# Performance work log

Hardware: AMD Instinct MI355X
Metric: run time of the kernel (lower is better)

Reference implementation:

```python
import jax, jax.numpy as jnp
import numpy as np

NEG_SLOPE = 0.2  # PyG GATConv default leaky_relu slope


def _gat_layer(x, src, dst, N, W, a_src, a_dst, b):
    # x: [N, Fin] -> h: [N, Fout]
    h = x @ W
    e_src = h @ a_src  # [N]
    e_dst = h @ a_dst  # [N]
    # per-edge attention logit, edge j->i uses src=j, dst=i
    e = jax.nn.leaky_relu(e_src[src] + e_dst[dst], NEG_SLOPE)  # [E]
    # segment softmax over incoming edges of each dst node
    m = jax.ops.segment_max(e, dst, num_segments=N)            # [N]
    ex = jnp.exp(e - m[dst])
    denom = jax.ops.segment_sum(ex, dst, num_segments=N)       # [N]
    alpha = ex / denom[dst]                                    # [E]
    out = jax.ops.segment_sum(alpha[:, None] * h[src], dst, num_segments=N)
    return out + b


def setup_inputs() -> dict:
    key = jax.random.key(0)
    ks = jax.random.split(key, 10)
    N, E_CNT, F_IN, F_HID, F_OUT = 100000, 3200000, 512, 8, 32
    E = jax.random.randint(ks[0], (2, E_CNT), 0, N, dtype=jnp.int64)
    X = jax.random.normal(ks[1], (N, F_IN), dtype=jnp.float32)
    s = 0.05
    return {
        "V": N,
        "E": E,
        "X": X,
        "W1": jax.random.normal(ks[2], (F_IN, F_HID), jnp.float32) * s,
        "a1_src": jax.random.normal(ks[3], (F_HID,), jnp.float32) * s,
        "a1_dst": jax.random.normal(ks[4], (F_HID,), jnp.float32) * s,
        "b1": jnp.zeros((F_HID,), jnp.float32),
        "W2": jax.random.normal(ks[5], (F_HID, F_OUT), jnp.float32) * s,
        "a2_src": jax.random.normal(ks[6], (F_OUT,), jnp.float32) * s,
        "a2_dst": jax.random.normal(ks[7], (F_OUT,), jnp.float32) * s,
        "b2": jnp.zeros((F_OUT,), jnp.float32),
    }


def reference(V, E, X, W1, a1_src, a1_dst, b1, W2, a2_src, a2_dst, b2):
    N = X.shape[0]
    # add_self_loops=True inside each GATConv
    loops = jnp.arange(N, dtype=E.dtype)
    src = jnp.concatenate([E[0], loops])
    dst = jnp.concatenate([E[1], loops])
    # dropout(p=0.6) is identity in eval mode
    h1 = jax.nn.elu(_gat_layer(X, src, dst, N, W1, a1_src, a1_dst, b1))
    out = _gat_layer(h1, src, dst, N, W2, a2_src, a2_dst, b2)
    return out
```

## Files before the change

kernel.cpp:

```cpp
#include <hip/hip_runtime.h>
#include <hip/hip_fp16.h>
#include <math.h>

#define F_IN 512
#define NEG_SLOPE 0.2f
#define CAPG 10240
#define SCAT_BLKS 768
#define CHUNK_MAX 4304
#define GEMM_BLKS 1536
#define NBUK_MAX 400

#define STG_OFF  0
#define LCNT_OFF (CHUNK_MAX)
#define LOFS_OFF (LCNT_OFF + 400)
#define GOFS_OFF (LOFS_OFF + 404)
#define WS_OFF   (GOFS_OFF + 400)
#define SMEM_INTS (WS_OFF + 8)

template <int CTRL>
__device__ __forceinline__ float dpp_row_add(float v) {
    int t = __builtin_amdgcn_update_dpp(0, __float_as_int(v), CTRL, 0xF, 0xF, true);
    return v + __int_as_float(t);
}
__device__ __forceinline__ float reduce16(float v) {
    v = dpp_row_add<0xB1>(v);
    v = dpp_row_add<0x4E>(v);
    v = dpp_row_add<0x124>(v);
    v = dpp_row_add<0x128>(v);
    return v;
}

__global__ __launch_bounds__(256) void k_main(
    const float* __restrict__ X, const float* __restrict__ W1,
    const float* __restrict__ a1s, const float* __restrict__ a1d,
    const float* __restrict__ W2, const float* __restrict__ a2s,
    const float* __restrict__ a2d,
    const int* __restrict__ E, int EC, int N,
    int* __restrict__ cursor, unsigned* __restrict__ bucketArr,
    char* __restrict__ rec1, float* __restrict__ e1d,
    float* __restrict__ wa2s, float* __restrict__ wa2d)
{
    __shared__ __align__(16) int smem[SMEM_INTS];
    int tid = threadIdx.x;
    int lane = tid & 63;
    int wv = tid >> 6;

    if (blockIdx.x < SCAT_BLKS) {
        unsigned* stage = (unsigned*)(smem + STG_OFF);
        int* lcnt = smem + LCNT_OFF;
        int* lofs = smem + LOFS_OFF;
        int* gofs = smem + GOFS_OFF;
        int* wsum = smem + WS_OFF;

        int odd = E[2 * lane + 1];
        unsigned long long bl = __ballot(odd == 0);
        int w64 = (bl == ~0ULL) ? 1 : 0;
        const int* srcBase = E;
        const int* dstBase = w64 ? (E + 2 * (size_t)EC) : (E + (size_t)EC);
        int step = w64 ? 2 : 1;
        int total = EC + N;
        int nb = (N + 255) >> 8;
        int chunk = (total + SCAT_BLKS - 1) / SCAT_BLKS;
        int e0 = blockIdx.x * chunk;
        int e1 = min(e0 + chunk, total);
        int cnt = max(e1 - e0, 0);

        for (int i = tid; i < NBUK_MAX; i += 256) lcnt[i] = 0;
        __syncthreads();
        for (int e = e0 + tid; e < e1; e += 256) {
            int d = (e < EC) ? dstBase[(size_t)e * step] : (e - EC);
            atomicAdd(&lcnt[d >> 8], 1);
        }
        __syncthreads();
        int b0 = tid * 2;
        int s0 = (b0 < nb) ? lcnt[b0] : 0;
        int s1 = (b0 + 1 < nb) ? lcnt[b0 + 1] : 0;
        int tsum = s0 + s1;
        int sc = tsum;
#pragma unroll
        for (int off = 1; off < 64; off <<= 1) {
            int t = __shfl_up(sc, off, 64);
            if (lane >= off) sc += t;
        }
        if (lane == 63) wsum[wv] = sc;
        __syncthreads();
        if (tid == 0) { int run = 0; for (int i = 0; i < 4; ++i) { int t = wsum[i]; wsum[i] = run; run += t; } }
        __syncthreads();
        int texc = wsum[wv] + sc - tsum;
        if (b0 < nb) lofs[b0] = texc;
        if (b0 + 1 < nb) lofs[b0 + 1] = texc + s0;
        if (tid == 0) lofs[nb] = cnt;
        __syncthreads();
        for (int b = tid; b < nb; b += 256) {
            int c = lcnt[b];
            gofs[b] = (c ? atomicAdd(&cursor[b], c) : 0) - lofs[b];
        }
        __syncthreads();
        for (int i = tid; i < NBUK_MAX; i += 256) lcnt[i] = 0;
        __syncthreads();
        for (int e = e0 + tid; e < e1; e += 256) {
            int s, d;
            if (e < EC) { s = srcBase[(size_t)e * step]; d = dstBase[(size_t)e * step]; }
            else        { s = e - EC; d = s; }
            int b = d >> 8;
            int r = atomicAdd(&lcnt[b], 1);
            stage[lofs[b] + r] = ((unsigned)(d & 255) << 24) | (unsigned)s;
        }
        __syncthreads();
        int WIN = (cnt + 3) >> 2;
        int wstart = wv * WIN;
        int wend = min(wstart + WIN, cnt);
        int i = wstart + lane;
        int p = 0;
        if (i < wend) {
            int lo = 0, hi = nb - 1;
            while (lo < hi) {
                int mid = (lo + hi + 1) >> 1;
                if (lofs[mid] <= i) lo = mid; else hi = mid - 1;
            }
            p = lo;
        }
        for (; i < wend; i += 64) {
            while (p + 1 < nb && lofs[p + 1] <= i) ++p;
            bucketArr[(size_t)p * CAPG + gofs[p] + i] = stage[i];
        }
    } else if (blockIdx.x < SCAT_BLKS + GEMM_BLKS) {
        float* rw = (float*)smem + wv * 680;

        float Wk[8][8];
        const float4* W4 = (const float4*)W1;
#pragma unroll
        for (int i = 0; i < 8; ++i) {
            int k = lane + 64 * i;
            float4 w0 = W4[k * 2], w1 = W4[k * 2 + 1];
            Wk[i][0]=w0.x; Wk[i][1]=w0.y; Wk[i][2]=w0.z; Wk[i][3]=w0.w;
            Wk[i][4]=w1.x; Wk[i][5]=w1.y; Wk[i][6]=w1.z; Wk[i][7]=w1.w;
        }
        float was[8], wad[8];
#pragma unroll
        for (int i = 0; i < 8; ++i) {
            float ts = 0.f, td = 0.f;
#pragma unroll
            for (int j = 0; j < 8; ++j) { ts += Wk[i][j] * a1s[j]; td += Wk[i][j] * a1d[j]; }
            was[i] = ts; wad[i] = td;
        }

        const int stride = GEMM_BLKS * 4;
        int row = (blockIdx.x - SCAT_BLKS) * 4 + wv;
        if (row >= N) return;
        float x[8], xn[8];
        {
            const float* xr = X + (size_t)row * F_IN + lane;
#pragma unroll
            for (int i = 0; i < 8; ++i) x[i] = xr[64 * i];
        }
        int j10 = lane & 15, c16 = lane >> 4;
        while (row < N) {
            int nrow = row + stride;
            if (nrow < N) {
                const float* xq = X + (size_t)nrow * F_IN + lane;
#pragma unroll
                for (int i = 0; i < 8; ++i) xn[i] = xq[64 * i];
            }
            float acc[8];
#pragma unroll
            for (int j = 0; j < 8; ++j) {
                float t = x[0] * Wk[0][j];
#pragma unroll
                for (int i = 1; i < 8; ++i) t += x[i] * Wk[i][j];
                acc[j] = t;
            }
            float accs = 0.f, accd = 0.f;
#pragma unroll
            for (int i = 0; i < 8; ++i) { accs += x[i] * was[i]; accd += x[i] * wad[i]; }
#pragma unroll
            for (int j = 0; j < 8; ++j) rw[j * 68 + lane] = acc[j];
            rw[8 * 68 + lane] = accs;
            rw[9 * 68 + lane] = accd;
            float s = 0.f;
            if (j10 < 10) {
                const float4* pr = (const float4*)&rw[j10 * 68 + c16 * 16];
                float4 q0 = pr[0], q1 = pr[1], q2 = pr[2], q3 = pr[3];
                s = ((q0.x+q0.y)+(q0.z+q0.w)) + ((q1.x+q1.y)+(q1.z+q1.w))
                  + ((q2.x+q2.y)+(q2.z+q2.w)) + ((q3.x+q3.y)+(q3.z+q3.w));
            }
            s += __shfl_xor(s, 16, 64);
            s += __shfl_xor(s, 32, 64);
            float hp = __shfl_xor(s, 1, 64);
            if (lane < 10) {
                char* rp = rec1 + (size_t)row * 32;
                if (lane < 8) {
                    if ((lane & 1) == 0)
                        *(__half2*)(rp + (lane >> 1) * 4) = __floats2half2_rn(s, hp);
                } else if (lane == 8) {
                    *(float*)(rp + 16) = s;
                } else {
                    e1d[row] = s;
                }
            }
            row = nrow;
#pragma unroll
            for (int i = 0; i < 8; ++i) x[i] = xn[i];
        }
    } else {
        if (tid < 8) {
            float s = 0.f;
            for (int j = 0; j < 32; ++j) s += W2[tid * 32 + j] * a2s[j];
            wa2s[tid] = s;
        } else if (tid < 16) {
            int k = tid - 8;
            float s = 0.f;
            for (int j = 0; j < 32; ++j) s += W2[k * 32 + j] * a2d[j];
            wa2d[k] = s;
        }
    }
}

__global__ __launch_bounds__(256) void k_csr_build(
    unsigned* __restrict__ bucketArr, const int* __restrict__ cursor,
    int2* __restrict__ offs2, int N)
{
    __shared__ int deg[256];
    __shared__ int wsum[4];
    __shared__ int stage[CAPG];
    int b = blockIdx.x;
    unsigned* ba = bucketArr + (size_t)b * CAPG;
    int cnt = min(cursor[b], CAPG);
    int bbase = b * CAPG;
    int nodeBase = b << 8;
    int nNodes = min(256, N - nodeBase);
    int tid = threadIdx.x;
    deg[tid] = 0;
    __syncthreads();
    for (int e = tid; e < cnt; e += 256)
        atomicAdd(&deg[ba[e] >> 24], 1);
    __syncthreads();
    int lane = tid & 63, wid = tid >> 6;
    int v = deg[tid];
    int s = v;
#pragma unroll
    for (int off = 1; off < 64; off <<= 1) {
        int t = __shfl_up(s, off, 64);
        if (lane >= off) s += t;
    }
    if (lane == 63) wsum[wid] = s;
    __syncthreads();
    if (tid == 0) { int run = 0; for (int i = 0; i < 4; ++i) { int t = wsum[i]; wsum[i] = run; run += t; } }
    __syncthreads();
    int ex = wsum[wid] + s - v;
    if (tid < nNodes) offs2[nodeBase + tid] = make_int2(bbase + ex, bbase + ex + v);
    __syncthreads();
    deg[tid] = ex;
    __syncthreads();
    for (int e = tid; e < cnt; e += 256) {
        unsigned pv = ba[e];
        int pos = atomicAdd(&deg[pv >> 24], 1);
        stage[pos] = (int)(pv & 0xFFFFFFu);
    }
    __syncthreads();
    for (int e = tid; e < cnt; e += 256)
        ba[e] = (unsigned)stage[e];
}

__global__ __launch_bounds__(256) void k_agg1(
    const int2* __restrict__ offs2, const unsigned* __restrict__ csr,
    const char* __restrict__ rec1, const float* __restrict__ e1d,
    const float* __restrict__ b1, const float* __restrict__ wa2s,
    const float* __restrict__ wa2d,
    char* __restrict__ rec2, float* __restrict__ e2d, int N)
{
    __shared__ float sb1[8], sws[8], swd[8];
    if (threadIdx.x < 8) sb1[threadIdx.x] = b1[threadIdx.x];
    else if (threadIdx.x < 16) sws[threadIdx.x - 8] = wa2s[threadIdx.x - 8];
    else if (threadIdx.x < 24) swd[threadIdx.x - 16] = wa2d[threadIdx.x - 16];
    __syncthreads();

    int lane = threadIdx.x & 63;
    int sub = (lane & 15) | ((lane >> 5) << 4);
    int g = (lane >> 4) & 1;
    int n = blockIdx.x * 8 + ((threadIdx.x >> 6) << 1) + g;
    if (n >= N) return;

    int2 be = offs2[n];
    int beg = be.x, end = be.y;
    float edn = e1d[n];
    float den = 0.f;
    float acc[8];
#pragma unroll
    for (int k = 0; k < 8; ++k) acc[k] = 0.f;

    for (int e = beg + sub; e < end; e += 32) {
        int s = (int)csr[e];
        const char* rp = rec1 + (size_t)s * 32;
        uint4 u = *(const uint4*)rp;
        float esv = *(const float*)(rp + 16);
        float t = esv + edn;
        t = fmaxf(t, NEG_SLOPE * t);
        float ex = __expf(fminf(t, 80.f));
        den += ex;
        float2 f0 = __half22float2(*(__half2*)&u.x);
        float2 f1 = __half22float2(*(__half2*)&u.y);
        float2 f2 = __half22float2(*(__half2*)&u.z);
        float2 f3 = __half22float2(*(__half2*)&u.w);
        acc[0] += ex * f0.x; acc[1] += ex * f0.y; acc[2] += ex * f1.x; acc[3] += ex * f1.y;
        acc[4] += ex * f2.x; acc[5] += ex * f2.y; acc[6] += ex * f3.x; acc[7] += ex * f3.y;
    }
    den = reduce16(den); den += __shfl_xor(den, 32, 64);
#pragma unroll
    for (int k = 0; k < 8; ++k) {
        acc[k] = reduce16(acc[k]);
        acc[k] += __shfl_xor(acc[k], 32, 64);
    }

    float inv = 1.f / den;
    float o[8]; float s2 = 0.f, d2 = 0.f;
#pragma unroll
    for (int k = 0; k < 8; ++k) {
        float t = acc[k] * inv + sb1[k];
        t = t > 0.f ? t : expm1f(t);
        o[k] = t; s2 += t * sws[k]; d2 += t * swd[k];
    }
    if (sub == 0) {
        __half2 p0 = __floats2half2_rn(o[0], o[1]);
        __half2 p1 = __floats2half2_rn(o[2], o[3]);
        __half2 p2 = __floats2half2_rn(o[4], o[5]);
        __half2 p3 = __floats2half2_rn(o[6], o[7]);
        uint4 u; u.x = *(unsigned*)&p0; u.y = *(unsigned*)&p1;
                 u.z = *(unsigned*)&p2; u.w = *(unsigned*)&p3;
        char* rp = rec2 + (size_t)n * 32;
        *(uint4*)rp = u;
        *(float*)(rp + 16) = s2;
        e2d[n] = d2;
    }
}

__global__ __launch_bounds__(256) void k_agg2(
    const int2* __restrict__ offs2, const unsigned* __restrict__ csr,
    const char* __restrict__ rec2, const float* __restrict__ e2d,
    const float* __restrict__ W2, const float* __restrict__ b2,
    float* __restrict__ out, int N)
{
    __shared__ float sW[256], sb[32];
    sW[threadIdx.x] = W2[threadIdx.x];
    if (threadIdx.x < 32) sb[threadIdx.x] = b2[threadIdx.x];
    __syncthreads();

    int lane = threadIdx.x & 63;
    int sub = (lane & 15) | ((lane >> 5) << 4);
    int g = (lane >> 4) & 1;
    int n = blockIdx.x * 8 + ((threadIdx.x >> 6) << 1) + g;
    if (n >= N) return;

    int2 be = offs2[n];
    int beg = be.x, end = be.y;
    float edn = e2d[n];
    float den = 0.f;
    float acc[8];
#pragma unroll
    for (int k = 0; k < 8; ++k) acc[k] = 0.f;

    for (int e = beg + sub; e < end; e += 32) {
        int s = (int)csr[e];
        const char* rp = rec2 + (size_t)s * 32;
        uint4 u = *(const uint4*)rp;
        float esv = *(const float*)(rp + 16);
        float t = esv + edn;
        t = fmaxf(t, NEG_SLOPE * t);
        float ex = __expf(fminf(t, 80.f));
        den += ex;
        float2 f0 = __half22float2(*(__half2*)&u.x);
        float2 f1 = __half22float2(*(__half2*)&u.y);
        float2 f2 = __half22float2(*(__half2*)&u.z);
        float2 f3 = __half22float2(*(__half2*)&u.w);
        acc[0] += ex * f0.x; acc[1] += ex * f0.y; acc[2] += ex * f1.x; acc[3] += ex * f1.y;
        acc[4] += ex * f2.x; acc[5] += ex * f2.y; acc[6] += ex * f3.x; acc[7] += ex * f3.y;
    }
    den = reduce16(den); den += __shfl_xor(den, 32, 64);
#pragma unroll
    for (int k = 0; k < 8; ++k) {
        acc[k] = reduce16(acc[k]);
        acc[k] += __shfl_xor(acc[k], 32, 64);
    }

    float inv = 1.f / den;
    float o = 0.f;
#pragma unroll
    for (int k = 0; k < 8; ++k) o += (acc[k] * inv) * sW[k * 32 + sub];
    out[(size_t)n * 32 + sub] = o + sb[sub];
}

extern "C" void kernel_launch(void* const* d_in, const int* in_sizes, int n_in,
                              void* d_out, int out_size, void* d_ws, size_t ws_size,
                              hipStream_t stream)
{
    const int*   E   = (const int*)d_in[1];
    const float* X   = (const float*)d_in[2];
    const float* W1  = (const float*)d_in[3];
    const float* a1s = (const float*)d_in[4];
    const float* a1d = (const float*)d_in[5];
    const float* b1  = (const float*)d_in[6];
    const float* W2  = (const float*)d_in[7];
    const float* a2s = (const float*)d_in[8];
    const float* a2d = (const float*)d_in[9];
    const float* b2  = (const float*)d_in[10];

    int N  = in_sizes[2] / F_IN;
    int EC = in_sizes[1] / 2;
    int NB = (N + 255) >> 8;

    char* w = (char*)d_ws;
    auto take = [&](size_t bytes) { char* p = w; w += (bytes + 255) & ~(size_t)255; return p; };

    char*  rec1 = take((size_t)N * 32);
    char*  rec2 = take((size_t)N * 32);
    float* e1d  = (float*)take((size_t)N * 4);
    float* e2d  = (float*)take((size_t)N * 4);
    unsigned* bucketArr = (unsigned*)take((size_t)NBUK_MAX * CAPG * 4);
    int2*  offs2 = (int2*)take((size_t)N * 8);
    int*   cursor = (int*)take(NBUK_MAX * 4);
    float* wa2s = (float*)take(256);
    float* wa2d = (float*)take(256);

    (void)hipMemsetAsync(cursor, 0, NBUK_MAX * 4, stream);

    k_main<<<SCAT_BLKS + GEMM_BLKS + 1, 256, 0, stream>>>(
        X, W1, a1s, a1d, W2, a2s, a2d, E, EC, N,
        cursor, bucketArr, rec1, e1d, wa2s, wa2d);

    k_csr_build<<<NB, 256, 0, stream>>>(bucketArr, cursor, offs2, N);

    int blocks8 = (N + 7) / 8;
    k_agg1<<<blocks8, 256, 0, stream>>>(offs2, bucketArr, rec1, e1d, b1, wa2s, wa2d,
                                        rec2, e2d, N);
    k_agg2<<<blocks8, 256, 0, stream>>>(offs2, bucketArr, rec2, e2d, W2, b2,
                                        (float*)d_out, N);
}
```

Baseline: 161.2 us.

## Fuse CSR build with layer-1 aggregation using shared-memory staged edges

The CSR build kernel and the layer-1 aggregation kernel are merged into one 512-thread kernel per 256-node bucket. After sorting edges into shared memory, each node is aggregated by a pair of threads that read source ids straight from the shared stage buffer. This removes a kernel launch and the global re-read of CSR indices and offsets. In exchange, parallelism per node drops from 32 lanes to 2, so high-degree nodes and load imbalance could lengthen the aggregation phase, and occupancy is limited by the large shared buffer.

```diff
diff --git a/kernel.cpp b/kernel.cpp
--- a/kernel.cpp
+++ b/kernel.cpp
@@ -216,13 +216,19 @@
     }
 }
 
-__global__ __launch_bounds__(256) void k_csr_build(
+__global__ __launch_bounds__(512) void k_csr_agg1(
     unsigned* __restrict__ bucketArr, const int* __restrict__ cursor,
-    int2* __restrict__ offs2, int N)
+    int2* __restrict__ offs2,
+    const char* __restrict__ rec1, const float* __restrict__ e1d,
+    const float* __restrict__ b1, const float* __restrict__ wa2s,
+    const float* __restrict__ wa2d,
+    char* __restrict__ rec2, float* __restrict__ e2d, int N)
 {
     __shared__ int deg[256];
+    __shared__ int begS[256];
     __shared__ int wsum[4];
     __shared__ int stage[CAPG];
+    __shared__ float sb1[8], sws[8], swd[8];
     int b = blockIdx.x;
     unsigned* ba = bucketArr + (size_t)b * CAPG;
     int cnt = min(cursor[b], CAPG);
@@ -230,103 +236,91 @@
     int nodeBase = b << 8;
     int nNodes = min(256, N - nodeBase);
     int tid = threadIdx.x;
-    deg[tid] = 0;
-    __syncthreads();
-    for (int e = tid; e < cnt; e += 256)
+
+    if (tid < 256) deg[tid] = 0;
+    else if (tid < 264) sb1[tid - 256] = b1[tid - 256];
+    else if (tid < 272) sws[tid - 264] = wa2s[tid - 264];
+    else if (tid < 280) swd[tid - 272] = wa2d[tid - 272];
+    __syncthreads();
+    for (int e = tid; e < cnt; e += 512)
         atomicAdd(&deg[ba[e] >> 24], 1);
     __syncthreads();
     int lane = tid & 63, wid = tid >> 6;
-    int v = deg[tid];
-    int s = v;
-#pragma unroll
-    for (int off = 1; off < 64; off <<= 1) {
-        int t = __shfl_up(s, off, 64);
-        if (lane >= off) s += t;
-    }
-    if (lane == 63) wsum[wid] = s;
+    int v = 0, s = 0;
+    if (tid < 256) {
+        v = deg[tid];
+        s = v;
+#pragma unroll
+        for (int off = 1; off < 64; off <<= 1) {
+            int t = __shfl_up(s, off, 64);
+            if (lane >= off) s += t;
+        }
+        if (lane == 63) wsum[wid] = s;
+    }
     __syncthreads();
     if (tid == 0) { int run = 0; for (int i = 0; i < 4; ++i) { int t = wsum[i]; wsum[i] = run; run += t; } }
     __syncthreads();
-    int ex = wsum[wid] + s - v;
-    if (tid < nNodes) offs2[nodeBase + tid] = make_int2(bbase + ex, bbase + ex + v);
-    __syncthreads();
-    deg[tid] = ex;
-    __syncthreads();
-    for (int e = tid; e < cnt; e += 256) {
+    if (tid < 256) {
+        int ex = wsum[wid] + s - v;
+        begS[tid] = ex;
+        if (tid < nNodes) offs2[nodeBase + tid] = make_int2(bbase + ex, bbase + ex + v);
+    }
+    __syncthreads();
+    if (tid < 256) deg[tid] = begS[tid];
+    __syncthreads();
+    for (int e = tid; e < cnt; e += 512) {
         unsigned pv = ba[e];
         int pos = atomicAdd(&deg[pv >> 24], 1);
         stage[pos] = (int)(pv & 0xFFFFFFu);
     }
     __syncthreads();
-    for (int e = tid; e < cnt; e += 256)
+    for (int e = tid; e < cnt; e += 512)
         ba[e] = (unsigned)stage[e];
-}
-
-__global__ __launch_bounds__(256) void k_agg1(
-    const int2* __restrict__ offs2, const unsigned* __restrict__ csr,
-    const char* __restrict__ rec1, const float* __restrict__ e1d,
-    const float* __restrict__ b1, const float* __restrict__ wa2s,
-    const float* __restrict__ wa2d,
-    char* __restrict__ rec2, float* __restrict__ e2d, int N)
-{
-    __shared__ float sb1[8], sws[8], swd[8];
-    if (threadIdx.x < 8) sb1[threadIdx.x] = b1[threadIdx.x];
-    else if (threadIdx.x < 16) sws[threadIdx.x - 8] = wa2s[threadIdx.x - 8];
-    else if (threadIdx.x < 24) swd[threadIdx.x - 16] = wa2d[threadIdx.x - 16];
-    __syncthreads();
-
-    int lane = threadIdx.x & 63;
-    int sub = (lane & 15) | ((lane >> 5) << 4);
-    int g = (lane >> 4) & 1;
-    int n = blockIdx.x * 8 + ((threadIdx.x >> 6) << 1) + g;
-    if (n >= N) return;
-
-    int2 be = offs2[n];
-    int beg = be.x, end = be.y;
-    float edn = e1d[n];
+    int node = tid >> 1, half = tid & 1;
     float den = 0.f;
     float acc[8];
 #pragma unroll
     for (int k = 0; k < 8; ++k) acc[k] = 0.f;
-
-    for (int e = beg + sub; e < end; e += 32) {
-        int s = (int)csr[e];
-        const char* rp = rec1 + (size_t)s * 32;
-        uint4 u = *(const uint4*)rp;
-        float esv = *(const float*)(rp + 16);
-        float t = esv + edn;
-        t = fmaxf(t, NEG_SLOPE * t);
-        float ex = __expf(fminf(t, 80.f));
-        den += ex;
-        float2 f0 = __half22float2(*(__half2*)&u.x);
-        float2 f1 = __half22float2(*(__half2*)&u.y);
-        float2 f2 = __half22float2(*(__half2*)&u.z);
-        float2 f3 = __half22float2(*(__half2*)&u.w);
-        acc[0] += ex * f0.x; acc[1] += ex * f0.y; acc[2] += ex * f1.x; acc[3] += ex * f1.y;
-        acc[4] += ex * f2.x; acc[5] += ex * f2.y; acc[6] += ex * f3.x; acc[7] += ex * f3.y;
-    }
-    den = reduce16(den); den += __shfl_xor(den, 32, 64);
-#pragma unroll
-    for (int k = 0; k < 8; ++k) {
-        acc[k] = reduce16(acc[k]);
-        acc[k] += __shfl_xor(acc[k], 32, 64);
-    }
-
-    float inv = 1.f / den;
-    float o[8]; float s2 = 0.f, d2 = 0.f;
-#pragma unroll
-    for (int k = 0; k < 8; ++k) {
-        float t = acc[k] * inv + sb1[k];
-        t = t > 0.f ? t : expm1f(t);
-        o[k] = t; s2 += t * sws[k]; d2 += t * swd[k];
-    }
-    if (sub == 0) {
+    if (node < nNodes) {
+        int beg = begS[node], end = deg[node];
+        float edn = e1d[nodeBase + node];
+        for (int e = beg + half; e < end; e += 2) {
+            int src = stage[e];
+            const char* rp = rec1 + (size_t)src * 32;
+            uint4 u = *(const uint4*)rp;
+            float esv = *(const float*)(rp + 16);
+            float t = esv + edn;
+            t = fmaxf(t, NEG_SLOPE * t);
+            float ex = __expf(fminf(t, 80.f));
+            den += ex;
+            float2 f0 = __half22float2(*(__half2*)&u.x);
+            float2 f1 = __half22float2(*(__half2*)&u.y);
+            float2 f2 = __half22float2(*(__half2*)&u.z);
+            float2 f3 = __half22float2(*(__half2*)&u.w);
+            acc[0] += ex * f0.x; acc[1] += ex * f0.y; acc[2] += ex * f1.x; acc[3] += ex * f1.y;
+            acc[4] += ex * f2.x; acc[5] += ex * f2.y; acc[6] += ex * f3.x; acc[7] += ex * f3.y;
+        }
+    }
+    den += __shfl_xor(den, 1, 64);
+#pragma unroll
+    for (int k = 0; k < 8; ++k) acc[k] += __shfl_xor(acc[k], 1, 64);
+
+    if (node < nNodes && half == 0) {
+        float inv = 1.f / den;
+        float o[8]; float s2 = 0.f, d2 = 0.f;
+#pragma unroll
+        for (int k = 0; k < 8; ++k) {
+            float t = acc[k] * inv + sb1[k];
+            t = t > 0.f ? t : expm1f(t);
+            o[k] = t; s2 += t * sws[k]; d2 += t * swd[k];
+        }
         __half2 p0 = __floats2half2_rn(o[0], o[1]);
         __half2 p1 = __floats2half2_rn(o[2], o[3]);
         __half2 p2 = __floats2half2_rn(o[4], o[5]);
         __half2 p3 = __floats2half2_rn(o[6], o[7]);
         uint4 u; u.x = *(unsigned*)&p0; u.y = *(unsigned*)&p1;
                  u.z = *(unsigned*)&p2; u.w = *(unsigned*)&p3;
+        int n = nodeBase + node;
         char* rp = rec2 + (size_t)n * 32;
         *(uint4*)rp = u;
         *(float*)(rp + 16) = s2;
@@ -427,11 +421,11 @@
         X, W1, a1s, a1d, W2, a2s, a2d, E, EC, N,
         cursor, bucketArr, rec1, e1d, wa2s, wa2d);
 
-    k_csr_build<<<NB, 256, 0, stream>>>(bucketArr, cursor, offs2, N);
+    k_csr_agg1<<<NB, 512, 0, stream>>>(bucketArr, cursor, offs2,
+                                       rec1, e1d, b1, wa2s, wa2d,
+                                       rec2, e2d, N);
 
     int blocks8 = (N + 7) / 8;
-    k_agg1<<<blocks8, 256, 0, stream>>>(offs2, bucketArr, rec1, e1d, b1, wa2s, wa2d,
-                                        rec2, e2d, N);
     k_agg2<<<blocks8, 256, 0, stream>>>(offs2, bucketArr, rec2, e2d, W2, b2,
                                         (float*)d_out, N);
 }
```

After: 138.2 us (median of 2 runs). 1.17x faster.
